# Kernel tuning notes

Hardware: AMD Instinct MI355X
Metric: run time of the kernel (lower is better)

The kernel has to match this reference:

```python
import jax, jax.numpy as jnp
import numpy as np

T, D, TR, CC, L = 4096, 512, 64, 64, 3  # time, input_size, trace, context, num_blocks


def setup_inputs() -> dict:
    key = jax.random.key(0)
    ks = jax.random.split(key, 10)
    x = jax.random.normal(ks[0], (T, D), dtype=jnp.float32)
    state = jnp.zeros((L, 1, TR, CC), dtype=jnp.float32)  # initial recurrent state (real part; imag is 0)
    start = jax.random.uniform(ks[1], (T,)) < 0.02  # episode-reset mask
    Wtr = jax.random.normal(ks[2], (L, TR, D), dtype=jnp.float32) / np.float32(np.sqrt(D))
    Wc = jax.random.normal(ks[3], (L, TR, D), dtype=jnp.float32) / np.float32(np.sqrt(D))
    a = jax.random.uniform(ks[4], (L, TR), minval=1e-6, maxval=0.1)
    b = 2 * jnp.pi / jnp.exp(jax.random.uniform(ks[5], (L, CC), minval=0.0, maxval=float(np.log(10000.0))))
    F = 2 * TR * CC
    W0 = jax.random.normal(ks[6], (L, D, F), dtype=jnp.float32) * np.float32(0.01 / np.sqrt(F))  # default_init scale=0.01
    b0 = jnp.zeros((L, D)); g0 = jnp.ones((L, D)); beta0 = jnp.zeros((L, D))
    W1 = jax.random.normal(ks[7], (L, D, D), dtype=jnp.float32) / np.float32(np.sqrt(D))
    b1 = jnp.zeros((L, D)); g1 = jnp.ones((L, D)); beta1 = jnp.zeros((L, D))
    return dict(x=x, state=state, start=start, Wtr=Wtr, Wc=Wc, a=a, b=b,
                W0=W0, b0=b0, g0=g0, beta0=beta0, W1=W1, b1=b1, g1=g1, beta1=beta1)


def _layernorm(z, g, b):
    m = jnp.mean(z, axis=-1, keepdims=True)
    v = jnp.mean((z - m) ** 2, axis=-1, keepdims=True)
    return (z - m) / jnp.sqrt(v + 1e-5) * g + b


def _sffm(x, st0, start, Wtr, Wc, a, b, W0, b0, g0, bb0, W1, b1, g1, bb1):
    t_len = x.shape[0]
    tr = x @ Wtr.T           # [T, TR]
    ct = x @ Wc.T            # [T, CC] (context proj also has trace_size outputs)
    pre = jnp.abs(tr[:, :, None] * ct[:, None, :])            # [T, TR, CC]
    pre = pre / (1e-8 + jnp.sum(pre, axis=(-2, -1), keepdims=True))
    # complex decay per (trace, context) pair: exp((-|a| + i b) * dt)
    ab = (-jnp.abs(a))[:, None] + 1j * b[None, :]             # [TR, CC] complex64

    def combine(carry, inc):
        ps, s, i = carry
        st, xx, j = inc
        s = s * jnp.logical_not(st)                            # reset gating
        dt = (j - i).astype(jnp.float32)[:, None, None]
        new = s * jnp.exp(ab[None] * dt) + xx
        return (jnp.logical_or(st, ps), new, j)

    ts = jnp.arange(t_len + 1, dtype=jnp.int32)
    sb = jnp.concatenate([jnp.zeros((1, 1, 1), bool), start.reshape(t_len, 1, 1)], axis=0)
    xs = jnp.concatenate([st0.astype(jnp.complex64), pre.astype(jnp.complex64)], axis=0)
    _, ns, _ = jax.lax.associative_scan(combine, (sb, xs, ts), axis=0)
    ns = ns[1:]                                                # [T, TR, CC] complex

    s = ns.reshape(t_len, TR * CC)
    mag = jnp.log1p(jnp.abs(s))
    ang = jnp.angle(s)
    scaled = jnp.concatenate([mag * jnp.sin(ang), mag * jnp.cos(ang)], axis=-1)  # [T, 2*TR*CC]
    z = jax.nn.leaky_relu(_layernorm(scaled @ W0.T + b0, g0, bb0))
    z = jax.nn.leaky_relu(_layernorm(z @ W1.T + b1, g1, bb1))
    return z


def reference(x, state, start, Wtr, Wc, a, b, W0, b0, g0, beta0, W1, b1, g1, beta1):
    z = x
    for l in range(L):
        z = _sffm(x, state[l], start, Wtr[l], Wc[l], a[l], b[l],
                  W0[l], b0[l], g0[l], beta0[l], W1[l], b1[l], g1[l], beta1[l])
        x = x + z
    return z  # NSFFM returns the last block's y
```

## Files before the change

### kernel.cpp

```cpp
#include <hip/hip_runtime.h>
#include <hip/hip_bf16.h>
#include <math.h>

#define T_LEN 4096
#define D_DIM 512
#define F_DIM 8192
#define NCHUNK 64
#define CLEN 64

typedef short short8 __attribute__((ext_vector_type(8)));
typedef float f32x4 __attribute__((ext_vector_type(4)));
typedef unsigned short u16;
typedef unsigned int u32;

__device__ inline float wave_sum(float v) {
#pragma unroll
  for (int o = 32; o; o >>= 1) v += __shfl_xor(v, o);
  return v;
}

__device__ inline u16 f2bf_bits(float v) {
  __hip_bfloat16 h = __float2bfloat16(v);
  return *(u16*)&h;
}

__device__ inline float bf2f(u16 u) {
  u32 x = ((u32)u) << 16;
  return *(float*)&x;
}

__device__ inline void gl_lds16(const void* g, void* l) {
  __builtin_amdgcn_global_load_lds((const __attribute__((address_space(1))) void*)g,
                                   (__attribute__((address_space(3))) void*)l, 16, 0, 0);
}

__global__ void detect_start(const unsigned char* __restrict__ s8, int* __restrict__ mode) {
  __shared__ int found;
  if (threadIdx.x == 0) found = 0;
  __syncthreads();
  for (int i = threadIdx.x; i < 4096; i += 256)
    if ((i & 3) && s8[i]) found = 1;
  __syncthreads();
  if (threadIdx.x == 0) mode[0] = found;
}

__device__ inline int read_start(const unsigned char* s8, const int* s32, int mode, int t) {
  return mode ? (int)s8[t] : s32[t];
}

__global__ void f2bf(const float* __restrict__ s, u16* __restrict__ d, int n) {
  int i = blockIdx.x * 256 + threadIdx.x;
  if (i < n) d[i] = f2bf_bits(s[i]);
}

__global__ void k_conv(const float* __restrict__ wtr, const float* __restrict__ wc,
                       u16* __restrict__ wcat, const float* __restrict__ w0,
                       u16* __restrict__ w0bf) {
  int i = blockIdx.x * 256 + threadIdx.x;
  if (i < 128 * D_DIM) {
    float v = (i < 64 * D_DIM) ? wtr[i] : wc[i - 64 * D_DIM];
    wcat[i] = f2bf_bits(v);
  }
  int j = i - 128 * D_DIM;
  if (j >= 0 && j < D_DIM * F_DIM) {
    int d = j >> 13, f = j & 8191;
    int r = f >> 7, rem = f & 127;
    int c = rem >> 1, b = rem & 1;
    float v = w0[(size_t)d * 8192 + b * 4096 + r * 64 + c];
    w0bf[(size_t)d * 8192 + (f ^ ((d & 7) << 3))] = f2bf_bits(v);
  }
}

template <int BM, int BN, int WR, int WC>
__global__ __launch_bounds__(256) void gemm_bt(const u16* __restrict__ A,
                                               const u16* __restrict__ B,
                                               float* __restrict__ C, int M, int N, int K) {
  constexpr int BK = 32;
  constexpr int MT = BM / (WR * 16);
  constexpr int NT = BN / (WC * 16);
  constexpr int AG = BM / 64;
  constexpr int BG = BN / 64;
  __shared__ u16 sA[BM * BK];
  __shared__ u16 sB[BN * BK];
  const int m0 = blockIdx.x * BM;
  const int n0 = blockIdx.y * BN;
  const int tid = threadIdx.x;
  const int wave = tid >> 6;
  const int lane = tid & 63;
  const int wr = wave / WC;
  const int wc = wave % WC;
  const int row_l = tid >> 2;
  const int c8 = (tid & 3) << 3;
  const int frow = lane & 15;
  const int fcol = (lane >> 4) << 3;

  f32x4 acc[MT][NT];
#pragma unroll
  for (int i = 0; i < MT; ++i)
#pragma unroll
    for (int j = 0; j < NT; ++j) acc[i][j] = (f32x4){0.f, 0.f, 0.f, 0.f};

  for (int k0 = 0; k0 < K; k0 += BK) {
#pragma unroll
    for (int j = 0; j < AG; ++j) {
      uint4 v = *(const uint4*)(A + (size_t)(m0 + j * 64 + row_l) * K + (k0 + c8));
      *(uint4*)(sA + (j * 64 + row_l) * BK + c8) = v;
    }
#pragma unroll
    for (int j = 0; j < BG; ++j) {
      uint4 v = *(const uint4*)(B + (size_t)(n0 + j * 64 + row_l) * K + (k0 + c8));
      *(uint4*)(sB + (j * 64 + row_l) * BK + c8) = v;
    }
    __syncthreads();
    short8 af[MT], bfr[NT];
#pragma unroll
    for (int i = 0; i < MT; ++i)
      af[i] = *(const short8*)(sA + (wr * MT * 16 + i * 16 + frow) * BK + fcol);
#pragma unroll
    for (int j = 0; j < NT; ++j)
      bfr[j] = *(const short8*)(sB + (wc * NT * 16 + j * 16 + frow) * BK + fcol);
#pragma unroll
    for (int i = 0; i < MT; ++i)
#pragma unroll
      for (int j = 0; j < NT; ++j)
        acc[i][j] = __builtin_amdgcn_mfma_f32_16x16x32_bf16(af[i], bfr[j], acc[i][j], 0, 0, 0);
    __syncthreads();
  }
#pragma unroll
  for (int i = 0; i < MT; ++i) {
    const int rbase = m0 + wr * MT * 16 + i * 16 + ((lane >> 4) << 2);
#pragma unroll
    for (int j = 0; j < NT; ++j) {
      const int col = n0 + wc * NT * 16 + j * 16 + (lane & 15);
#pragma unroll
      for (int rg = 0; rg < 4; ++rg) C[(size_t)(rbase + rg) * N + col] = acc[i][j][rg];
    }
  }
}

__global__ __launch_bounds__(256) void gemm128(const u16* __restrict__ A,
                                               const u16* __restrict__ B,
                                               u16* __restrict__ Cp, size_t pstride, int N,
                                               int Ktot) {
  __shared__ u16 sA[128 * 64];
  __shared__ u16 sB[128 * 64];
  const int tid = threadIdx.x;
  const int wave = tid >> 6;
  const int lane = tid & 63;
  const int wr = wave >> 1;
  const int wc = wave & 1;
  const int m0 = blockIdx.x * 128;
  const int n0 = blockIdx.y * 128;
  const int ks = blockIdx.z;
  const int Kper = Ktot / gridDim.z;
  const int kb = ks * Kper;
  const int row_s = tid >> 3;
  const int g8 = (tid & 7) << 3;
  const int frow = lane & 15;
  const int quad = lane >> 4;
  const int sw = frow & 7;

  f32x4 acc[4][4];
#pragma unroll
  for (int i = 0; i < 4; ++i)
#pragma unroll
    for (int j = 0; j < 4; ++j) acc[i][j] = (f32x4){0.f, 0.f, 0.f, 0.f};

  for (int k0 = kb; k0 < kb + Kper; k0 += 64) {
#pragma unroll
    for (int j = 0; j < 4; ++j) {
      gl_lds16(A + (size_t)(m0 + j * 32 + row_s) * Ktot + (k0 + g8), sA + j * 2048 + wave * 512);
      gl_lds16(B + (size_t)(n0 + j * 32 + row_s) * Ktot + (k0 + g8), sB + j * 2048 + wave * 512);
    }
    asm volatile("s_waitcnt vmcnt(0)" ::: "memory");
    __syncthreads();
#pragma unroll
    for (int kk = 0; kk < 2; ++kk) {
      const int gA = (((kk << 2) | quad) ^ sw) << 3;
      short8 af[4], bfr[4];
#pragma unroll
      for (int i = 0; i < 4; ++i)
        af[i] = *(const short8*)(sA + (wr * 64 + i * 16 + frow) * 64 + gA);
#pragma unroll
      for (int j = 0; j < 4; ++j)
        bfr[j] = *(const short8*)(sB + (wc * 64 + j * 16 + frow) * 64 + gA);
#pragma unroll
      for (int i = 0; i < 4; ++i)
#pragma unroll
        for (int j = 0; j < 4; ++j)
          acc[i][j] = __builtin_amdgcn_mfma_f32_16x16x32_bf16(af[i], bfr[j], acc[i][j], 0, 0, 0);
    }
    __syncthreads();
  }
#pragma unroll
  for (int i = 0; i < 4; ++i) {
    const int rbase = m0 + wr * 64 + i * 16 + ((lane >> 4) << 2);
#pragma unroll
    for (int j = 0; j < 4; ++j) {
      const int col = n0 + wc * 64 + j * 16 + (lane & 15);
#pragma unroll
      for (int rg = 0; rg < 4; ++rg)
        Cp[(size_t)ks * pstride + (size_t)(rbase + rg) * N + col] = f2bf_bits(acc[i][j][rg]);
    }
  }
}

__global__ __launch_bounds__(512, 2) void gemm_8ph(const u16* __restrict__ A,
                                                   const u16* __restrict__ B,
                                                   u16* __restrict__ Cp, size_t pstride, int N,
                                                   int Ktot) {
  extern __shared__ u16 smem[];
  u16* sA = smem;
  const int tid = threadIdx.x;
  const int wave = tid >> 6;
  const int lane = tid & 63;
  const int wr = wave >> 1;
  const int wc = wave & 1;
  const int m0 = blockIdx.x * 256;
  const int n0 = blockIdx.y * 128;
  const int ks = blockIdx.z;
  const int Kper = Ktot / gridDim.z;
  const int kb = ks * Kper;
  const int nT = Kper >> 6;
  const int r_l = tid >> 3;
  const int g8 = (tid & 7) << 3;
  const int frow = lane & 15;
  const int quad = lane >> 4;
  const int sw = frow & 7;
  const int o0 = (quad ^ sw) << 3;
  const int o1 = ((4 | quad) ^ sw) << 3;

  const u16* Abase = A + (size_t)(m0 + r_l) * Ktot + g8;
  const u16* Bbase = B + (size_t)(n0 + wc * 64 + frow) * (size_t)Ktot;

#define STAGE_A(l, k0, b) \
  gl_lds16(Abase + (size_t)(l) * 64 * Ktot + (k0), sA + (b)*16384 + (l)*4096 + wave * 512)
#define RD_A(dst, b, qm_)                                               \
  do {                                                                  \
    const u16* _p = sA + (b)*16384 + (wr * 64 + (qm_)*32 + frow) * 64;  \
    dst[0][0] = *(const short8*)(_p + o0);                              \
    dst[0][1] = *(const short8*)(_p + o1);                              \
    dst[1][0] = *(const short8*)(_p + 1024 + o0);                       \
    dst[1][1] = *(const short8*)(_p + 1024 + o1);                       \
  } while (0)
#define GLB_B(dst, half_)                                          \
  do {                                                             \
    const u16* _q = Bk + (size_t)((half_)*32) * Ktot;              \
    dst[0][0] = *(const short8*)(_q + o0);                         \
    dst[0][1] = *(const short8*)(_q + o1);                         \
    dst[1][0] = *(const short8*)(_q + (size_t)16 * Ktot + o0);     \
    dst[1][1] = *(const short8*)(_q + (size_t)16 * Ktot + o1);     \
  } while (0)

  f32x4 acc[4][4];
#pragma unroll
  for (int i = 0; i < 4; ++i)
#pragma unroll
    for (int j = 0; j < 4; ++j) acc[i][j] = (f32x4){0.f, 0.f, 0.f, 0.f};

  short8 af_lo[2][2];
  short8 af_hi[2][2];
  short8 bfr0[2][2];
  short8 bfr1[2][2];

  STAGE_A(0, kb, 0);
  STAGE_A(1, kb, 0);
  STAGE_A(2, kb, 0);
  STAGE_A(3, kb, 0);
  STAGE_A(0, kb + 64, 1);
  STAGE_A(1, kb + 64, 1);
  STAGE_A(2, kb + 64, 1);
  STAGE_A(3, kb + 64, 1);
  asm volatile("s_waitcnt vmcnt(4)" ::: "memory");
  __builtin_amdgcn_s_barrier();

  int bc = 0;
  for (int t = 0; t < nT; ++t) {
    const int k0 = kb + (t << 6);
    int bs = bc + 2;
    if (bs >= 3) bs -= 3;
    const bool nl = (t + 2 < nT);
    const u16* Bk = Bbase + k0;
    GLB_B(bfr0, 0);
    GLB_B(bfr1, 1);
    RD_A(af_lo, bc, 0);
    RD_A(af_hi, bc, 1);
    if (nl) {
      STAGE_A(0, k0 + 128, bs);
      STAGE_A(1, k0 + 128, bs);
      STAGE_A(2, k0 + 128, bs);
      STAGE_A(3, k0 + 128, bs);
    }
    if (nl)
      asm volatile("s_waitcnt vmcnt(4)" ::: "memory");
    else
      asm volatile("s_waitcnt vmcnt(0)" ::: "memory");
    asm volatile("s_waitcnt lgkmcnt(0)" ::: "memory");
    __builtin_amdgcn_sched_barrier(0);
    __builtin_amdgcn_s_setprio(1);
#pragma unroll
    for (int f = 0; f < 2; ++f)
#pragma unroll
      for (int g = 0; g < 2; ++g)
#pragma unroll
        for (int kk = 0; kk < 2; ++kk)
          acc[f][g] = __builtin_amdgcn_mfma_f32_16x16x32_bf16(af_lo[f][kk], bfr0[g][kk],
                                                              acc[f][g], 0, 0, 0);
#pragma unroll
    for (int f = 0; f < 2; ++f)
#pragma unroll
      for (int g = 0; g < 2; ++g)
#pragma unroll
        for (int kk = 0; kk < 2; ++kk)
          acc[f][2 + g] = __builtin_amdgcn_mfma_f32_16x16x32_bf16(af_lo[f][kk], bfr1[g][kk],
                                                                  acc[f][2 + g], 0, 0, 0);
#pragma unroll
    for (int f = 0; f < 2; ++f)
#pragma unroll
      for (int g = 0; g < 2; ++g)
#pragma unroll
        for (int kk = 0; kk < 2; ++kk)
          acc[2 + f][2 + g] = __builtin_amdgcn_mfma_f32_16x16x32_bf16(
              af_hi[f][kk], bfr1[g][kk], acc[2 + f][2 + g], 0, 0, 0);
#pragma unroll
    for (int f = 0; f < 2; ++f)
#pragma unroll
      for (int g = 0; g < 2; ++g)
#pragma unroll
        for (int kk = 0; kk < 2; ++kk)
          acc[2 + f][g] = __builtin_amdgcn_mfma_f32_16x16x32_bf16(af_hi[f][kk], bfr0[g][kk],
                                                                  acc[2 + f][g], 0, 0, 0);
    __builtin_amdgcn_s_setprio(0);
    __builtin_amdgcn_s_barrier();
    bc += 1;
    if (bc >= 3) bc -= 3;
  }
#undef STAGE_A
#undef RD_A
#undef GLB_B

#pragma unroll
  for (int i = 0; i < 4; ++i) {
    const int rbase = m0 + wr * 64 + i * 16 + (quad << 2);
#pragma unroll
    for (int j = 0; j < 4; ++j) {
      const int col = n0 + wc * 64 + j * 16 + frow;
#pragma unroll
      for (int rg = 0; rg < 4; ++rg)
        Cp[(size_t)ks * pstride + (size_t)(rbase + rg) * N + col] = f2bf_bits(acc[i][j][rg]);
    }
  }
}

__global__ void prep_pq(const float* __restrict__ trct, float* __restrict__ pT,
                        float* __restrict__ q) {
  int t = blockIdx.x;
  int lane = threadIdx.x;
  float tr = trct[t * 128 + lane];
  float ct = trct[t * 128 + 64 + lane];
  float ap = fabsf(tr), aq = fabsf(ct);
  float Sp = wave_sum(ap);
  float Sq = wave_sum(aq);
  float denom = 1e-8f + Sp * Sq;
  pT[lane * T_LEN + t] = ap;
  q[t * 64 + lane] = aq / denom;
}

__global__ void scan_phase1(const float* __restrict__ pT, const float* __restrict__ q,
                            const unsigned char* __restrict__ st8, const int* __restrict__ st32,
                            const int* __restrict__ modep, const float* __restrict__ a,
                            const float* __restrict__ b, float4* __restrict__ chunkbuf) {
  int chunk = blockIdx.x, r = blockIdx.y, c = threadIdx.x;
  int mode = modep[0];
  int t0 = chunk * CLEN;
  float na = -fabsf(a[r]);
  float rho = __expf(na);
  float bb = b[c];
  float er = rho * __cosf(bb), ei = rho * __sinf(bb);
  float pv = pT[r * T_LEN + t0 + c];
  int sv = read_start(st8, st32, mode, t0 + c);
  unsigned long long bal = __ballot(sv != 0);
  float Ar, Ai;
  if (bal) {
    Ar = 0.f; Ai = 0.f;
  } else {
    float mag = __expf(64.f * na);
    float ang = 64.f * bb;
    Ar = mag * __cosf(ang);
    Ai = mag * __sinf(ang);
  }
  int L = bal ? (63 - __builtin_clzll(bal)) : 0;
  float Br = 0.f, Bi = 0.f;
  const float* qrow = q + (size_t)t0 * 64 + c;
  for (int i = L; i < CLEN; ++i) {
    float pre = __shfl(pv, i) * qrow[i * 64];
    float nBr = er * Br - ei * Bi + pre;
    Bi = er * Bi + ei * Br;
    Br = nBr;
  }
  chunkbuf[((size_t)chunk * 64 + r) * 64 + c] = make_float4(Ar, Ai, Br, Bi);
}

__global__ void scan_phase2(const float4* __restrict__ chunkbuf, const float* __restrict__ state,
                            float2* __restrict__ s0buf) {
  int r = blockIdx.x, c = threadIdx.x;
  float Sr = state[r * 64 + c], Si = 0.f;
  for (int k = 0; k < NCHUNK; ++k) {
    s0buf[((size_t)k * 64 + r) * 64 + c] = make_float2(Sr, Si);
    float4 ab = chunkbuf[((size_t)k * 64 + r) * 64 + c];
    float nSr = ab.x * Sr - ab.y * Si + ab.z;
    Si = ab.x * Si + ab.y * Sr + ab.w;
    Sr = nSr;
  }
}

__global__ void scan_phase3(const float* __restrict__ pT, const float* __restrict__ q,
                            const unsigned char* __restrict__ st8, const int* __restrict__ st32,
                            const int* __restrict__ modep, const float* __restrict__ a,
                            const float* __restrict__ b, const float2* __restrict__ s0buf,
                            u32* __restrict__ scaled, int c0) {
  int chunk = c0 + blockIdx.x, r = blockIdx.y, c = threadIdx.x;
  int mode = modep[0];
  int t0 = chunk * CLEN;
  float rho = __expf(-fabsf(a[r]));
  float bb = b[c];
  float er = rho * __cosf(bb), ei = rho * __sinf(bb);
  float pv = pT[r * T_LEN + t0 + c];
  int sv = read_start(st8, st32, mode, t0 + c);
  float2 s0 = s0buf[((size_t)chunk * 64 + r) * 64 + c];
  float Sr = s0.x, Si = s0.y;
  int tl0 = (chunk - c0) * CLEN;
  const float* qrow = q + (size_t)t0 * 64 + c;
  u32* srow = scaled + (size_t)tl0 * 4096;
  const int Ldw = r * 64 + c;
#pragma unroll 4
  for (int i = 0; i < CLEN; ++i) {
    float qt = qrow[i * 64];
    float pt = __shfl(pv, i);
    int st = __shfl(sv, i);
    float pre = pt * qt;
    float cer = st ? 0.f : er;
    float cei = st ? 0.f : ei;
    float nSr = cer * Sr - cei * Si + pre;
    Si = cer * Si + cei * Sr;
    Sr = nSr;
    float m2 = fmaf(Sr, Sr, Si * Si);
    float rsq = rsqrtf(fmaxf(m2, 1e-30f));
    float m = m2 * rsq;
    float sc = __log2f(1.0f + m) * 0.6931471805599453f * rsq;
    u32 pack = ((u32)f2bf_bits(sc * Sr) << 16) | (u32)f2bf_bits(sc * Si);
    srow[(size_t)i * 4096 + (Ldw ^ ((i & 7) << 2))] = pack;
  }
}

__global__ void ln_act16(const u16* __restrict__ parts, int KS, size_t pstride,
                         const float* __restrict__ bias, const float* __restrict__ gam,
                         const float* __restrict__ bet, u16* __restrict__ zbf) {
  __shared__ float red[8];
  int t = blockIdx.x, tid = threadIdx.x;
  size_t o = (size_t)t * D_DIM + tid;
  float v0 = bias[tid];
  float v1 = bias[tid + 256];
  for (int ks = 0; ks < KS; ++ks) {
    v0 += bf2f(parts[(size_t)ks * pstride + o]);
    v1 += bf2f(parts[(size_t)ks * pstride + o + 256]);
  }
  float s = wave_sum(v0 + v1);
  if ((tid & 63) == 0) red[tid >> 6] = s;
  __syncthreads();
  float mean = (red[0] + red[1] + red[2] + red[3]) * (1.f / 512.f);
  float d0 = v0 - mean, d1 = v1 - mean;
  float s2 = wave_sum(d0 * d0 + d1 * d1);
  if ((tid & 63) == 0) red[4 + (tid >> 6)] = s2;
  __syncthreads();
  float var = (red[4] + red[5] + red[6] + red[7]) * (1.f / 512.f);
  float rstd = rsqrtf(var + 1e-5f);
  float z0 = d0 * rstd * gam[tid] + bet[tid];
  float z1 = d1 * rstd * gam[tid + 256] + bet[tid + 256];
  z0 = z0 > 0.f ? z0 : 0.01f * z0;
  z1 = z1 > 0.f ? z1 : 0.01f * z1;
  zbf[o] = f2bf_bits(z0);
  zbf[o + 256] = f2bf_bits(z1);
}

__global__ void ln_act32(const float* __restrict__ y, const float* __restrict__ bias,
                         const float* __restrict__ gam, const float* __restrict__ bet,
                         const float* __restrict__ xsrc, float* __restrict__ xdst,
                         u16* __restrict__ xbf_next, float* __restrict__ finout) {
  __shared__ float red[8];
  int t = blockIdx.x, tid = threadIdx.x;
  size_t o = (size_t)t * D_DIM + tid;
  float v0 = y[o] + bias[tid];
  float v1 = y[o + 256] + bias[tid + 256];
  float s = wave_sum(v0 + v1);
  if ((tid & 63) == 0) red[tid >> 6] = s;
  __syncthreads();
  float mean = (red[0] + red[1] + red[2] + red[3]) * (1.f / 512.f);
  float d0 = v0 - mean, d1 = v1 - mean;
  float s2 = wave_sum(d0 * d0 + d1 * d1);
  if ((tid & 63) == 0) red[4 + (tid >> 6)] = s2;
  __syncthreads();
  float var = (red[4] + red[5] + red[6] + red[7]) * (1.f / 512.f);
  float rstd = rsqrtf(var + 1e-5f);
  float z0 = d0 * rstd * gam[tid] + bet[tid];
  float z1 = d1 * rstd * gam[tid + 256] + bet[tid + 256];
  z0 = z0 > 0.f ? z0 : 0.01f * z0;
  z1 = z1 > 0.f ? z1 : 0.01f * z1;
  if (xdst) {
    float x0 = xsrc[o] + z0, x1 = xsrc[o + 256] + z1;
    xdst[o] = x0;
    xdst[o + 256] = x1;
    xbf_next[o] = f2bf_bits(x0);
    xbf_next[o + 256] = f2bf_bits(x1);
  }
  if (finout) {
    finout[o] = z0;
    finout[o + 256] = z1;
  }
}

__global__ void err_signal(float* __restrict__ out, float code) {
  if (threadIdx.x == 0) out[0] = code;
}

extern "C" void kernel_launch(void* const* d_in, const int* in_sizes, int n_in, void* d_out,
                              int out_size, void* d_ws, size_t ws_size, hipStream_t stream) {
  const float* x_in = (const float*)d_in[0];
  const float* state = (const float*)d_in[1];
  const unsigned char* start8 = (const unsigned char*)d_in[2];
  const int* start32 = (const int*)d_in[2];
  const float* Wtr = (const float*)d_in[3];
  const float* Wc = (const float*)d_in[4];
  const float* a_in = (const float*)d_in[5];
  const float* b_in = (const float*)d_in[6];
  const float* W0 = (const float*)d_in[7];
  const float* b0 = (const float*)d_in[8];
  const float* g0 = (const float*)d_in[9];
  const float* beta0 = (const float*)d_in[10];
  const float* W1 = (const float*)d_in[11];
  const float* b1 = (const float*)d_in[12];
  const float* g1 = (const float*)d_in[13];
  const float* beta1 = (const float*)d_in[14];
  float* out = (float*)d_out;

  static int attr_state = 0;
  if (attr_state == 0)
    attr_state = (hipFuncSetAttribute((const void*)gemm_8ph,
                                      hipFuncAttributeMaxDynamicSharedMemorySize,
                                      98304) == hipSuccess)
                     ? 1
                     : -1;
  const bool attr_ok = (attr_state == 1);

  char* w = (char*)d_ws;
  auto alloc = [&](size_t bytes) {
    char* ptr = w;
    w += (bytes + 255) & ~(size_t)255;
    return ptr;
  };
  float* x_ws = (float*)alloc(4ull * T_LEN * D_DIM);
  u16* xbf = (u16*)alloc(2ull * T_LEN * D_DIM);
  u16* wcat = (u16*)alloc(2ull * 128 * D_DIM);
  u16* w0bf = (u16*)alloc(2ull * D_DIM * F_DIM);
  u16* w1bf = (u16*)alloc(2ull * 3 * D_DIM * D_DIM);
  float* trct = (float*)alloc(4ull * T_LEN * 128);
  float* pTbuf = (float*)alloc(4ull * T_LEN * 64);
  float* qbuf = (float*)alloc(4ull * T_LEN * 64);
  float4* chunkbuf = (float4*)alloc(16ull * NCHUNK * 64 * 64);
  float2* s0buf = (float2*)alloc(8ull * NCHUNK * 64 * 64);
  u16* z0bf = (u16*)alloc(2ull * T_LEN * D_DIM);
  float* ybuf = (float*)alloc(4ull * T_LEN * D_DIM);
  int* modep = (int*)alloc(256);
  size_t base1 = (size_t)(w - (char*)d_ws);

  if (n_in != 15) {
    err_signal<<<1, 64, 0, stream>>>(out, 9e6f + 1000.f * n_in);
    return;
  }
  const size_t MB = 1ull << 20;
  const size_t pstride = (size_t)T_LEN * D_DIM;
  int KS, nseg;
  if (ws_size >= base1 + 16 * MB + 64 * MB) { KS = 4; nseg = 1; }
  else if (ws_size >= base1 + 16 * MB + 32 * MB) { KS = 4; nseg = 2; }
  else if (ws_size >= base1 + 8 * MB + 32 * MB) { KS = 2; nseg = 2; }
  else if (ws_size >= base1 + 8 * MB + 16 * MB) { KS = 2; nseg = 4; }
  else if (ws_size >= base1 + 4 * MB + 16 * MB) { KS = 1; nseg = 4; }
  else {
    err_signal<<<1, 64, 0, stream>>>(out, 9e6f);
    return;
  }
  const int seg_rows = T_LEN / nseg;
  const int seg_chunks = NCHUNK / nseg;
  u16* ypart = (u16*)alloc(2ull * KS * pstride);
  u16* scaled = (u16*)alloc(2ull * seg_rows * F_DIM);

  const bool use8 = (nseg == 1) && attr_ok;

  detect_start<<<1, 256, 0, stream>>>(start8, modep);
  f2bf<<<(T_LEN * D_DIM) / 256, 256, 0, stream>>>(x_in, xbf, T_LEN * D_DIM);
  f2bf<<<(3 * D_DIM * D_DIM) / 256, 256, 0, stream>>>(W1, w1bf, 3 * D_DIM * D_DIM);

  for (int l = 0; l < 3; ++l) {
    const float* Wtr_l = Wtr + (size_t)l * 64 * D_DIM;
    const float* Wc_l = Wc + (size_t)l * 64 * D_DIM;
    const float* a_l = a_in + l * 64;
    const float* b_l = b_in + l * 64;
    const float* W0_l = W0 + (size_t)l * D_DIM * F_DIM;
    const u16* w1bf_l = w1bf + (size_t)l * D_DIM * D_DIM;
    const float* state_l = state + (size_t)l * 64 * 64;
    const float* xsrc = (l == 0) ? x_in : x_ws;

    k_conv<<<(128 * D_DIM + D_DIM * F_DIM) / 256, 256, 0, stream>>>(Wtr_l, Wc_l, wcat, W0_l,
                                                                    w0bf);
    gemm_bt<64, 64, 2, 2><<<dim3(T_LEN / 64, 2), 256, 0, stream>>>(xbf, wcat, trct, T_LEN, 128,
                                                                   D_DIM);
    prep_pq<<<T_LEN, 64, 0, stream>>>(trct, pTbuf, qbuf);
    scan_phase1<<<dim3(NCHUNK, 64), 64, 0, stream>>>(pTbuf, qbuf, start8, start32, modep, a_l,
                                                     b_l, chunkbuf);
    scan_phase2<<<64, 64, 0, stream>>>(chunkbuf, state_l, s0buf);

    for (int h = 0; h < nseg; ++h) {
      scan_phase3<<<dim3(seg_chunks, 64), 64, 0, stream>>>(pTbuf, qbuf, start8, start32, modep,
                                                           a_l, b_l, s0buf, (u32*)scaled,
                                                           h * seg_chunks);
      if (use8)
        gemm_8ph<<<dim3(seg_rows / 256, D_DIM / 128, KS), 512, 98304, stream>>>(
            scaled, w0bf, ypart + (size_t)h * seg_rows * D_DIM, pstride, D_DIM, F_DIM);
      else
        gemm128<<<dim3(seg_rows / 128, D_DIM / 128, KS), 256, 0, stream>>>(
            scaled, w0bf, ypart + (size_t)h * seg_rows * D_DIM, pstride, D_DIM, F_DIM);
    }
    ln_act16<<<T_LEN, 256, 0, stream>>>(ypart, KS, pstride, b0 + l * D_DIM, g0 + l * D_DIM,
                                        beta0 + l * D_DIM, z0bf);
    gemm_bt<64, 64, 2, 2><<<dim3(T_LEN / 64, D_DIM / 64), 256, 0, stream>>>(z0bf, w1bf_l, ybuf,
                                                                            T_LEN, D_DIM, D_DIM);
    ln_act32<<<T_LEN, 256, 0, stream>>>(ybuf, b1 + l * D_DIM, g1 + l * D_DIM, beta1 + l * D_DIM,
                                        (l < 2) ? xsrc : nullptr, (l < 2) ? x_ws : nullptr,
                                        (l < 2) ? xbf : nullptr, (l == 2) ? out : nullptr);
  }
}
```

Before: 563.5 us.

## Double-buffer B register fragments and unroll GEMM K-loop by two

The GEMM main loop is unrolled by two and B fragments are prefetched from global memory into a second register set one K-tile ahead. Previously they were loaded and waited on in the same iteration. This is meant to hide global-load latency for B behind the MFMA work. The waitcnt thresholds are adjusted to match. It doubles B fragment register use, which may hurt occupancy, and it assumes nT is even.

```diff
diff --git a/kernel.cpp b/kernel.cpp
--- a/kernel.cpp
+++ b/kernel.cpp
@@ -235,6 +235,13 @@
 
 #define STAGE_A(l, k0, b) \
   gl_lds16(Abase + (size_t)(l) * 64 * Ktot + (k0), sA + (b)*16384 + (l)*4096 + wave * 512)
+#define STAGE4(k0, b)    \
+  do {                   \
+    STAGE_A(0, k0, b);   \
+    STAGE_A(1, k0, b);   \
+    STAGE_A(2, k0, b);   \
+    STAGE_A(3, k0, b);   \
+  } while (0)
 #define RD_A(dst, b, qm_)                                               \
   do {                                                                  \
     const u16* _p = sA + (b)*16384 + (wr * 64 + (qm_)*32 + frow) * 64;  \
@@ -243,14 +250,41 @@
     dst[1][0] = *(const short8*)(_p + 1024 + o0);                       \
     dst[1][1] = *(const short8*)(_p + 1024 + o1);                       \
   } while (0)
-#define GLB_B(dst, half_)                                          \
+#define GLB_B(d0_, d1_, kadd)                                      \
   do {                                                             \
-    const u16* _q = Bk + (size_t)((half_)*32) * Ktot;              \
-    dst[0][0] = *(const short8*)(_q + o0);                         \
-    dst[0][1] = *(const short8*)(_q + o1);                         \
-    dst[1][0] = *(const short8*)(_q + (size_t)16 * Ktot + o0);     \
-    dst[1][1] = *(const short8*)(_q + (size_t)16 * Ktot + o1);     \
+    const u16* _q = Bbase + (kadd);                                \
+    d0_[0][0] = *(const short8*)(_q + o0);                         \
+    d0_[0][1] = *(const short8*)(_q + o1);                         \
+    d0_[1][0] = *(const short8*)(_q + (size_t)16 * Ktot + o0);     \
+    d0_[1][1] = *(const short8*)(_q + (size_t)16 * Ktot + o1);     \
+    d1_[0][0] = *(const short8*)(_q + (size_t)32 * Ktot + o0);     \
+    d1_[0][1] = *(const short8*)(_q + (size_t)32 * Ktot + o1);     \
+    d1_[1][0] = *(const short8*)(_q + (size_t)48 * Ktot + o0);     \
+    d1_[1][1] = *(const short8*)(_q + (size_t)48 * Ktot + o1);     \
   } while (0)
+#define MFMA32(b0_, b1_)                                                                 \
+  do {                                                                                   \
+    _Pragma("unroll") for (int f = 0; f < 2; ++f)                                        \
+        _Pragma("unroll") for (int g = 0; g < 2; ++g)                                    \
+            _Pragma("unroll") for (int kk = 0; kk < 2; ++kk) acc[f][g] =                 \
+                __builtin_amdgcn_mfma_f32_16x16x32_bf16(af_lo[f][kk], b0_[g][kk],        \
+                                                        acc[f][g], 0, 0, 0);             \
+    _Pragma("unroll") for (int f = 0; f < 2; ++f)                                        \
+        _Pragma("unroll") for (int g = 0; g < 2; ++g)                                    \
+            _Pragma("unroll") for (int kk = 0; kk < 2; ++kk) acc[f][2 + g] =             \
+                __builtin_amdgcn_mfma_f32_16x16x32_bf16(af_lo[f][kk], b1_[g][kk],        \
+                                                        acc[f][2 + g], 0, 0, 0);         \
+    _Pragma("unroll") for (int f = 0; f < 2; ++f)                                        \
+        _Pragma("unroll") for (int g = 0; g < 2; ++g)                                    \
+            _Pragma("unroll") for (int kk = 0; kk < 2; ++kk) acc[2 + f][2 + g] =         \
+                __builtin_amdgcn_mfma_f32_16x16x32_bf16(af_hi[f][kk], b1_[g][kk],        \
+                                                        acc[2 + f][2 + g], 0, 0, 0);     \
+    _Pragma("unroll") for (int f = 0; f < 2; ++f)                                        \
+        _Pragma("unroll") for (int g = 0; g < 2; ++g)                                    \
+            _Pragma("unroll") for (int kk = 0; kk < 2; ++kk) acc[2 + f][g] =             \
+                __builtin_amdgcn_mfma_f32_16x16x32_bf16(af_hi[f][kk], b0_[g][kk],        \
+                                                        acc[2 + f][g], 0, 0, 0);         \
+  } while (0)
 
   f32x4 acc[4][4];
 #pragma unroll
@@ -258,86 +292,70 @@
 #pragma unroll
     for (int j = 0; j < 4; ++j) acc[i][j] = (f32x4){0.f, 0.f, 0.f, 0.f};
 
-  short8 af_lo[2][2];
-  short8 af_hi[2][2];
-  short8 bfr0[2][2];
-  short8 bfr1[2][2];
-
-  STAGE_A(0, kb, 0);
-  STAGE_A(1, kb, 0);
-  STAGE_A(2, kb, 0);
-  STAGE_A(3, kb, 0);
-  STAGE_A(0, kb + 64, 1);
-  STAGE_A(1, kb + 64, 1);
-  STAGE_A(2, kb + 64, 1);
-  STAGE_A(3, kb + 64, 1);
+  short8 af_lo[2][2], af_hi[2][2];
+  short8 bA0[2][2], bA1[2][2];
+  short8 bB0[2][2], bB1[2][2];
+
+  STAGE4(kb, 0);
+  GLB_B(bA0, bA1, kb);
+  STAGE4(kb + 64, 1);
+  __builtin_amdgcn_sched_barrier(0);
   asm volatile("s_waitcnt vmcnt(4)" ::: "memory");
   __builtin_amdgcn_s_barrier();
+  __builtin_amdgcn_sched_barrier(0);
 
   int bc = 0;
-  for (int t = 0; t < nT; ++t) {
+  for (int t = 0; t < nT; t += 2) {
     const int k0 = kb + (t << 6);
-    int bs = bc + 2;
-    if (bs >= 3) bs -= 3;
     const bool nl = (t + 2 < nT);
-    const u16* Bk = Bbase + k0;
-    GLB_B(bfr0, 0);
-    GLB_B(bfr1, 1);
+    int b1 = bc + 1;
+    if (b1 >= 3) b1 -= 3;
+    int b2 = bc + 2;
+    if (b2 >= 3) b2 -= 3;
+
     RD_A(af_lo, bc, 0);
     RD_A(af_hi, bc, 1);
+    GLB_B(bB0, bB1, k0 + 64);
+    if (nl) STAGE4(k0 + 128, b2);
+    __builtin_amdgcn_sched_barrier(0);
+    if (nl)
+      asm volatile("s_waitcnt vmcnt(12)" ::: "memory");
+    else
+      asm volatile("s_waitcnt vmcnt(8)" ::: "memory");
+    asm volatile("s_waitcnt lgkmcnt(0)" ::: "memory");
+    __builtin_amdgcn_sched_barrier(0);
+    __builtin_amdgcn_s_setprio(1);
+    MFMA32(bA0, bA1);
+    __builtin_amdgcn_s_setprio(0);
+    __builtin_amdgcn_s_barrier();
+    __builtin_amdgcn_sched_barrier(0);
+
+    RD_A(af_lo, b1, 0);
+    RD_A(af_hi, b1, 1);
     if (nl) {
-      STAGE_A(0, k0 + 128, bs);
-      STAGE_A(1, k0 + 128, bs);
-      STAGE_A(2, k0 + 128, bs);
-      STAGE_A(3, k0 + 128, bs);
-    }
+      GLB_B(bA0, bA1, k0 + 128);
+      STAGE4(k0 + 192, bc);
+    }
+    __builtin_amdgcn_sched_barrier(0);
     if (nl)
-      asm volatile("s_waitcnt vmcnt(4)" ::: "memory");
+      asm volatile("s_waitcnt vmcnt(12)" ::: "memory");
     else
       asm volatile("s_waitcnt vmcnt(0)" ::: "memory");
     asm volatile("s_waitcnt lgkmcnt(0)" ::: "memory");
     __builtin_amdgcn_sched_barrier(0);
     __builtin_amdgcn_s_setprio(1);
-#pragma unroll
-    for (int f = 0; f < 2; ++f)
-#pragma unroll
-      for (int g = 0; g < 2; ++g)
-#pragma unroll
-        for (int kk = 0; kk < 2; ++kk)
-          acc[f][g] = __builtin_amdgcn_mfma_f32_16x16x32_bf16(af_lo[f][kk], bfr0[g][kk],
-                                                              acc[f][g], 0, 0, 0);
-#pragma unroll
-    for (int f = 0; f < 2; ++f)
-#pragma unroll
-      for (int g = 0; g < 2; ++g)
-#pragma unroll
-        for (int kk = 0; kk < 2; ++kk)
-          acc[f][2 + g] = __builtin_amdgcn_mfma_f32_16x16x32_bf16(af_lo[f][kk], bfr1[g][kk],
-                                                                  acc[f][2 + g], 0, 0, 0);
-#pragma unroll
-    for (int f = 0; f < 2; ++f)
-#pragma unroll
-      for (int g = 0; g < 2; ++g)
-#pragma unroll
-        for (int kk = 0; kk < 2; ++kk)
-          acc[2 + f][2 + g] = __builtin_amdgcn_mfma_f32_16x16x32_bf16(
-              af_hi[f][kk], bfr1[g][kk], acc[2 + f][2 + g], 0, 0, 0);
-#pragma unroll
-    for (int f = 0; f < 2; ++f)
-#pragma unroll
-      for (int g = 0; g < 2; ++g)
-#pragma unroll
-        for (int kk = 0; kk < 2; ++kk)
-          acc[2 + f][g] = __builtin_amdgcn_mfma_f32_16x16x32_bf16(af_hi[f][kk], bfr0[g][kk],
-                                                                  acc[2 + f][g], 0, 0, 0);
+    MFMA32(bB0, bB1);
     __builtin_amdgcn_s_setprio(0);
     __builtin_amdgcn_s_barrier();
-    bc += 1;
-    if (bc >= 3) bc -= 3;
+    __builtin_amdgcn_sched_barrier(0);
+
+    bc = b2;
   }
 #undef STAGE_A
+#undef STAGE4
 #undef RD_A
 #undef GLB_B
+#undef MFMA32
 
 #pragma unroll
   for (int i = 0; i < 4; ++i) {
```

Measured after the change: 548.7 us. 2.6% less time.
